# Kernel tuning notes

Hardware: AMD Instinct MI355X
Metric: run time of the kernel (lower is better)

## Reference

```python
import jax, jax.numpy as jnp
import numpy as np

NE = 14          # NUM_ELEMENTS
NC = 20          # NUM_CHANNEL
DEN = NE         # density channel
GRV = NE + 1     # gravity channel

# (id, density, gravity) per element, in id order
_ELEMS = [(0,1,1),(1,4,0),(2,3,1),(3,2,1),(4,0,1),(5,4,0),(6,4,0),(7,0,1),(8,4,0),(9,3,1),(10,3,1),(11,2,1),(12,3,1),(13,4,0)]

def _elem_table():
    t = np.zeros((NE, NC), dtype=np.float32)
    for eid, dens, grav in _ELEMS:
        t[eid, eid] = 1.0
        t[eid, DEN] = dens
        t[eid, GRV] = grav
    return jnp.asarray(t)

# torch.roll semantics: get_above(x)[h] = x[h-1] (wrap)
above = lambda x: jnp.roll(x, 1, axis=2)
below = lambda x: jnp.roll(x, -1, axis=2)
left  = lambda x: jnp.roll(x, 1, axis=3)
right = lambda x: jnp.roll(x, -1, axis=3)

def interp2(sa, sb, if_false, if_a, if_b):
    # faithful to torch: (~a & ~b)*f + a*xa + b*xb (bools broadcast-multiply floats)
    return (jnp.logical_and(~sa, ~sb)) * if_false + sa * if_a + sb * if_b

def setup_inputs() -> dict:
    key = jax.random.key(0)
    k1, k2 = jax.random.split(key)
    B, H, W = 8, 512, 512
    ids = jax.random.randint(k1, (B, H, W), 0, NE)
    world = _elem_table()[ids]                 # [B,H,W,NC]
    world = jnp.transpose(world, (0, 3, 1, 2)) # [B,NC,H,W]
    rand_movement = jax.random.uniform(k2, (B, 1, H, W), dtype=jnp.float32)
    return {"world": world, "rand_movement": rand_movement}

def reference(world, rand_movement):
    B, C, H, W = world.shape
    # --- stone support check (conv2d with zero padding, taps at top-left/top-right) ---
    stone = world[:, 9:10]
    p = jnp.pad(stone, ((0, 0), (0, 0), (1, 1), (1, 1)))
    supports = p[:, :, 0:H, 0:W] + p[:, :, 0:H, 2:W + 2]  # stone[h-1,w-1]+stone[h-1,w+1]
    new_grav = (1.0 - stone) * world[:, GRV:GRV + 1] + stone * (supports < 2)
    world = world.at[:, GRV:GRV + 1].set(new_grav)

    # --- vertical gravity passes over densities 0..3 ---
    did_gravity = jnp.zeros((B, 1, H, W), dtype=world.dtype)
    for curr_density in (0, 1, 2, 3):
        density = world[:, DEN:DEN + 1]
        is_density_above_greater = (above(density) - density) > 0
        is_density_below_less = below(is_density_above_greater)
        is_density_current = density == curr_density
        is_density_above_current = above(is_density_current)
        is_gravity = world[:, GRV:GRV + 1] == 1
        is_cb_gravity = jnp.logical_and(below(is_gravity), is_gravity)
        is_ca_gravity = jnp.logical_and(above(is_gravity), is_gravity)
        does_become_below = is_density_current & is_density_below_less & is_cb_gravity
        does_become_above = is_density_above_greater & is_density_above_current & is_ca_gravity
        did_gravity = did_gravity + does_become_above
        world = interp2(does_become_below, does_become_above, world, below(world), above(world))

    # --- diagonal fall for sand (2) and dust (12) ---
    for elem in (2, 12):
        fall_dir = rand_movement > 0.5
        not_did_gravity = did_gravity <= 0
        for fall_left in (True, False):
            g_dir = left if fall_left else right
            g_not = right if fall_left else left
            is_element = world[:, elem:elem + 1] == 1
            is_ar_element = g_not(above(is_element))
            density = world[:, DEN:DEN + 1]
            is_matching_fall = fall_dir if fall_left else ~fall_dir
            is_ar_matching_fall = g_not(above(is_matching_fall))
            is_bl_density_lower = (density - g_dir(below(density))) > 0
            is_ar_density_higher = (g_not(above(density)) - density) > 0
            is_gravity = world[:, GRV:GRV + 1] == 1
            is_bl_gravity = jnp.logical_and(g_dir(below(is_gravity)), is_gravity)
            is_ar_gravity = jnp.logical_and(g_not(above(is_gravity)), is_gravity)
            ndg_bl = jnp.logical_and(g_dir(below(not_did_gravity)), not_did_gravity)
            ndg_ar = jnp.logical_and(g_not(above(not_did_gravity)), not_did_gravity)
            does_become_bl = is_element & ndg_bl & is_matching_fall & is_bl_density_lower & is_bl_gravity
            does_become_ar = is_ar_element & ndg_ar & is_ar_matching_fall & is_ar_density_higher & is_ar_gravity
            world = interp2(does_become_bl, does_become_ar, world, g_dir(below(world)), g_not(above(world)))
    return world
```

## Files before the change

kernel.cpp:

```cpp
#include <hip/hip_runtime.h>
#include <stdint.h>

#define HH 512
#define WW 512
#define PLANE (HH*WW)
#define NCH 20

#define GRAV_PACK 0x1E9Du

__device__ __forceinline__ void bar_lds() {
    __builtin_amdgcn_sched_barrier(0);
    asm volatile("s_waitcnt lgkmcnt(0)" ::: "memory");
    __builtin_amdgcn_s_barrier();
    __builtin_amdgcn_sched_barrier(0);
}

__device__ __forceinline__ uint32_t eqz4(uint32_t x) {
    uint32_t nz = (x | (x >> 1) | (x >> 2) | (x >> 3)) & 0x01010101u;
    return nz ^ 0x01010101u;
}
__device__ __forceinline__ uint32_t bmask(uint32_t b) {
    uint32_t h = b << 7;
    return (h - (h >> 7)) | h;
}

__device__ __forceinline__ uint32_t pack_cell(float d_,
                                              float c1_, float c5_, float c6_, float c8_,
                                              float c2_, float c9_, float c10_,
                                              float c3_, float c4_) {
    int d = (int)d_;
    int e;
    if (d == 4)      e = (c1_ != 0.f) ? 1 : (c5_ != 0.f) ? 5 : (c6_ != 0.f) ? 6 : (c8_ != 0.f) ? 8 : 13;
    else if (d == 3) e = (c2_ != 0.f) ? 2 : (c9_ != 0.f) ? 9 : (c10_ != 0.f) ? 10 : 12;
    else if (d == 2) e = (c3_ != 0.f) ? 3 : 11;
    else if (d == 1) e = 0;
    else             e = (c4_ != 0.f) ? 4 : 7;
    int g = (int)((GRAV_PACK >> e) & 1u);
    return (uint32_t)(e | (g << 4) | (d << 5));
}

__global__ __launch_bounds__(256) void extract_k(const float* __restrict__ world,
                                                 uint32_t* __restrict__ st) {
    int idx = blockIdx.x * 256 + threadIdx.x;
    int b  = idx >> 16;
    int p4 = idx & 0xFFFF;
    const float4* base = (const float4*)(world + (size_t)b * NCH * PLANE) + p4;
    float4 vD  = base[14 * (PLANE / 4)];
    float4 v1  = base[ 1 * (PLANE / 4)];
    float4 v5  = base[ 5 * (PLANE / 4)];
    float4 v6  = base[ 6 * (PLANE / 4)];
    float4 v8  = base[ 8 * (PLANE / 4)];
    float4 v2  = base[ 2 * (PLANE / 4)];
    float4 v9  = base[ 9 * (PLANE / 4)];
    float4 v10 = base[10 * (PLANE / 4)];
    float4 v3  = base[ 3 * (PLANE / 4)];
    float4 v4  = base[ 4 * (PLANE / 4)];
    uint32_t b0 = pack_cell(vD.x, v1.x, v5.x, v6.x, v8.x, v2.x, v9.x, v10.x, v3.x, v4.x);
    uint32_t b1 = pack_cell(vD.y, v1.y, v5.y, v6.y, v8.y, v2.y, v9.y, v10.y, v3.y, v4.y);
    uint32_t b2 = pack_cell(vD.z, v1.z, v5.z, v6.z, v8.z, v2.z, v9.z, v10.z, v3.z, v4.z);
    uint32_t b3 = pack_cell(vD.w, v1.w, v5.w, v6.w, v8.w, v2.w, v9.w, v10.w, v3.w, v4.w);
    st[idx] = b0 | (b1 << 8) | (b2 << 16) | (b3 << 24);
}

#define TILE_R 32
#define TILE_C 64
#define HALO_T 9
#define HALO_B 8
#define HALO_W 8
#define RH (TILE_R + HALO_T + HALO_B)
#define RWW 20
#define RWS 21
#define NW (RH*RWW)
#define NT 512
#define NOWN 2

__global__ __launch_bounds__(NT, 4) void sim_k(const uint8_t* __restrict__ st_in,
                                               const float* __restrict__ rnd,
                                               float* __restrict__ out) {
    __shared__ uint32_t bufA[RH * RWS];
    __shared__ uint32_t bufB[RH * RWS];
    __shared__ uint32_t aux [RH * RWS];

    const int tid = threadIdx.x;
    const int h0  = blockIdx.y * TILE_R;
    const int w0  = blockIdx.x * TILE_C;

    uint32_t sreg[NOWN], freg[NOWN], dgreg[NOWN];

    auto stage = [&](const uint8_t* stb, const float* rb) {
#pragma unroll
        for (int k = 0; k < NOWN; ++k) {
            int r = tid + k * NT;
            if (r < NW) {
                int i = r / RWW, jw = r - i * RWW;
                int gh  = (h0 + i - HALO_T) & (HH - 1);
                int gwb = (w0 + jw * 4 - HALO_W) & (WW - 1);
                uint32_t w = *(const uint32_t*)(stb + gh * WW + gwb);
                bufA[i * RWS + jw] = w;
                sreg[k] = w;
                float4 rv = *(const float4*)(rb + gh * WW + gwb);
                uint32_t aw = 0;
                aw |= (rv.x > 0.5f) ? 0x00000001u : 0u;
                aw |= (rv.y > 0.5f) ? 0x00000100u : 0u;
                aw |= (rv.z > 0.5f) ? 0x00010000u : 0u;
                aw |= (rv.w > 0.5f) ? 0x01000000u : 0u;
                freg[k] = aw;
                dgreg[k] = 0u;
            }
        }
    };

    auto passes = [&]() {
#pragma unroll
        for (int k = 0; k < NOWN; ++k) {
            int r = tid + k * NT;
            if (r < NW) {
                int i = r / RWW, jw = r - i * RWW;
                uint32_t s = sreg[k];
                uint32_t stm = eqz4((s & 0x0F0F0F0Fu) ^ 0x09090909u);
                int im = (i > 0) ? i - 1 : 0;
                int jl = (jw > 0) ? jw - 1 : 0;
                int jr = (jw < RWW - 1) ? jw + 1 : RWW - 1;
                uint32_t wU  = bufA[im * RWS + jw];
                uint32_t wUL = bufA[im * RWS + jl];
                uint32_t wUR = bufA[im * RWS + jr];
                uint32_t upL = (wU << 8) | (wUL >> 24);
                uint32_t upR = (wU >> 8) | (wUR << 24);
                uint32_t stL = eqz4((upL & 0x0F0F0F0Fu) ^ 0x09090909u);
                uint32_t stR = eqz4((upR & 0x0F0F0F0Fu) ^ 0x09090909u);
                int gh  = (h0 + i - HALO_T) & (HH - 1);
                int gwb = (w0 + jw * 4 - HALO_W) & (WW - 1);
                uint32_t rowOK = (gh != 0) ? 0x01010101u : 0u;
                uint32_t okL = 0x01010101u ^ ((gwb == 0)      ? 0x00000001u : 0u);
                uint32_t okR = 0x01010101u ^ ((gwb == WW - 4) ? 0x01000000u : 0u);
                uint32_t supL = stL & okL & rowOK;
                uint32_t supR = stR & okR & rowOK;
                uint32_t g2 = 0x01010101u ^ (supL & supR);
                uint32_t ns = (s & ~0x10101010u) | (g2 << 4);
                uint32_t res = s ^ ((s ^ ns) & bmask(stm));
                bufB[i * RWS + jw] = res;
                sreg[k] = res;
            }
        }
        bar_lds();

        uint32_t* cur = bufB;
        uint32_t* nxt = bufA;

#pragma unroll
        for (int curr = 0; curr < 4; ++curr) {
            const uint32_t crep = (uint32_t)curr * 0x01010101u;
            const uint32_t CKP7 = crep + 0x0F0F0F0Fu;
#pragma unroll
            for (int k = 0; k < NOWN; ++k) {
                int r = tid + k * NT;
                if (r < NW) {
                    int i = r / RWW, jw = r - i * RWW;
                    int ia = (i > 0) ? i - 1 : 0;
                    int ib = (i < RH - 1) ? i + 1 : RH - 1;
                    uint32_t s  = sreg[k];
                    uint32_t sa = cur[ia * RWS + jw];
                    uint32_t sb = cur[ib * RWS + jw];
                    uint32_t d  = (s  >> 5) & 0x07070707u;
                    uint32_t da = (sa >> 5) & 0x07070707u;
                    uint32_t db = (sb >> 5) & 0x07070707u;
                    uint32_t g  = (s  >> 4) & 0x01010101u;
                    uint32_t ga = (sa >> 4) & 0x01010101u;
                    uint32_t gb = (sb >> 4) & 0x01010101u;
                    uint32_t bel = eqz4(d ^ crep)  & (((CKP7 - db) & 0x10101010u) >> 4) & gb & g;
                    uint32_t abv = eqz4(da ^ crep) & (((CKP7 - d)  & 0x10101010u) >> 4) & ga & g;
                    uint32_t res = s ^ ((s ^ sb) & bmask(bel)) ^ ((s ^ sa) & bmask(abv));
                    nxt[i * RWS + jw] = res;
                    sreg[k] = res;
                    dgreg[k] |= abv;
                    if (curr == 3)
                        aux[i * RWS + jw] = freg[k] | (dgreg[k] << 1);
                }
            }
            bar_lds();
            uint32_t* t = cur; cur = nxt; nxt = t;
        }

#pragma unroll
        for (int pass = 0; pass < 4; ++pass) {
            const int  elem = (pass < 2) ? 2 : 12;
            const bool fl   = ((pass & 1) == 0);
            const uint32_t erep = (uint32_t)elem * 0x01010101u;
#pragma unroll
            for (int k = 0; k < NOWN; ++k) {
                int r = tid + k * NT;
                if (r < NW) {
                    int i = r / RWW, jw = r - i * RWW;
                    int ia = (i > 0) ? i - 1 : 0;
                    int ib = (i < RH - 1) ? i + 1 : RH - 1;
                    int jl = (jw > 0) ? jw - 1 : 0;
                    int jr = (jw < RWW - 1) ? jw + 1 : RWW - 1;
                    uint32_t s  = sreg[k];
                    uint32_t wB = cur[ib * RWS + jw];
                    uint32_t wA = cur[ia * RWS + jw];
                    uint32_t aB = aux[ib * RWS + jw];
                    uint32_t aA = aux[ia * RWS + jw];
                    uint32_t sbl, sar, abl, aar;
                    if (fl) {
                        uint32_t wBL = cur[ib * RWS + jl], wAR = cur[ia * RWS + jr];
                        uint32_t aBL = aux[ib * RWS + jl], aAR = aux[ia * RWS + jr];
                        sbl = (wB << 8) | (wBL >> 24);
                        sar = (wA >> 8) | (wAR << 24);
                        abl = (aB << 8) | (aBL >> 24);
                        aar = (aA >> 8) | (aAR << 24);
                    } else {
                        uint32_t wBR = cur[ib * RWS + jr], wAL = cur[ia * RWS + jl];
                        uint32_t aBR = aux[ib * RWS + jr], aAL = aux[ia * RWS + jl];
                        sbl = (wB >> 8) | (wBR << 24);
                        sar = (wA << 8) | (wAL >> 24);
                        abl = (aB >> 8) | (aBR << 24);
                        aar = (aA << 8) | (aAL >> 24);
                    }
                    uint32_t d   = (s   >> 5) & 0x07070707u;
                    uint32_t dbl = (sbl >> 5) & 0x07070707u;
                    uint32_t dar = (sar >> 5) & 0x07070707u;
                    uint32_t g   = (s   >> 4) & 0x01010101u;
                    uint32_t gbl = (sbl >> 4) & 0x01010101u;
                    uint32_t gar = (sar >> 4) & 0x01010101u;
                    uint32_t ndg   = dgreg[k] ^ 0x01010101u;
                    uint32_t ndgbl = ((~abl) >> 1) & 0x01010101u;
                    uint32_t ndgar = ((~aar) >> 1) & 0x01010101u;
                    uint32_t mtc = (fl ? freg[k] : ~freg[k]) & 0x01010101u;
                    uint32_t mta = (fl ? aar : ~aar) & 0x01010101u;
                    uint32_t eqe  = eqz4((s   & 0x0F0F0F0Fu) ^ erep);
                    uint32_t eqer = eqz4((sar & 0x0F0F0F0Fu) ^ erep);
                    uint32_t bbl = eqe  & ndgbl & ndg & mtc & (((0x12121212u - dbl) & 0x10101010u) >> 4) & gbl & g;
                    uint32_t bar = eqer & ndgar & ndg & mta & (((0x12121212u - d)   & 0x10101010u) >> 4) & gar & g;
                    uint32_t res = s ^ ((s ^ sbl) & bmask(bbl)) ^ ((s ^ sar) & bmask(bar));
                    nxt[i * RWS + jw] = res;
                    sreg[k] = res;
                }
            }
            bar_lds();
            uint32_t* t = cur; cur = nxt; nxt = t;
        }
    };

    auto expand = [&](float* ob, uint32_t w) {
        float* base = ob + (size_t)(h0 + (tid >> 4)) * WW + (w0 + (tid & 15) * 4);
        uint32_t oh0 = 1u << ( w        & 15u);
        uint32_t oh1 = 1u << ((w >>  8) & 15u);
        uint32_t oh2 = 1u << ((w >> 16) & 15u);
        uint32_t oh3 = 1u << ((w >> 24) & 15u);
#pragma unroll
        for (int c = 0; c < 14; ++c) {
            float4 v;
            v.x = (float)((oh0 >> c) & 1u);
            v.y = (float)((oh1 >> c) & 1u);
            v.z = (float)((oh2 >> c) & 1u);
            v.w = (float)((oh3 >> c) & 1u);
            *(float4*)(base + (size_t)c * PLANE) = v;
        }
        float4 vd = { (float)((w >>  5) & 7u), (float)((w >> 13) & 7u),
                      (float)((w >> 21) & 7u), (float)((w >> 29) & 7u) };
        *(float4*)(base + (size_t)14 * PLANE) = vd;
        float4 vg = { (float)((w >>  4) & 1u), (float)((w >> 12) & 1u),
                      (float)((w >> 20) & 1u), (float)((w >> 28) & 1u) };
        *(float4*)(base + (size_t)15 * PLANE) = vg;
        float4 z = {0.f, 0.f, 0.f, 0.f};
#pragma unroll
        for (int c = 16; c < 20; ++c)
            *(float4*)(base + (size_t)c * PLANE) = z;
    };

    const int bA = blockIdx.z, bB = blockIdx.z + 4;
    const uint8_t* stA = st_in + (size_t)bA * PLANE;
    const uint8_t* stB = st_in + (size_t)bB * PLANE;
    const float*   rA  = rnd   + (size_t)bA * PLANE;
    const float*   rB  = rnd   + (size_t)bB * PLANE;
    float* obA = out + (size_t)bA * NCH * PLANE;
    float* obB = out + (size_t)bB * NCH * PLANE;

    const int coreIdx = (HALO_T + (tid >> 4)) * RWS + (HALO_W / 4) + (tid & 15);

    stage(stA, rA);
    bar_lds();
    passes();

    uint32_t wA = bufB[coreIdx];
    stage(stB, rB);
    expand(obA, wA);
    bar_lds();
    passes();

    expand(obB, bufB[coreIdx]);
}

extern "C" void kernel_launch(void* const* d_in, const int* in_sizes, int n_in,
                              void* d_out, int out_size, void* d_ws, size_t ws_size,
                              hipStream_t stream) {
    const float* world = (const float*)d_in[0];
    const float* rnd   = (const float*)d_in[1];
    float* out = (float*)d_out;
    uint32_t* st = (uint32_t*)d_ws;

    extract_k<<<2048, 256, 0, stream>>>(world, st);

    dim3 grid(WW / TILE_C, HH / TILE_R, 4);
    sim_k<<<grid, NT, 0, stream>>>((const uint8_t*)st, rnd, out);
}
```

Before: 55.49 us.

## Fuse float-to-packed extraction into sim kernel and double tile height

Removes the separate extract kernel and its packed intermediate buffer. The sim kernel now reads the ten needed float channels directly from the world tensor during staging and packs them in-register. To reduce the redundant halo reads this causes (halo cells now cost ten float4 loads each), the tile height goes from 32 to 64 rows, with 4 owned words per thread and occupancy bounds lowered to 2 blocks per SIMD group. This saves one launch and a global round trip, but adds more global traffic per halo cell, more registers and fewer resident blocks.

After: 73.89 us. 1.33x slower.

```diff
diff --git a/kernel.cpp b/kernel.cpp
--- a/kernel.cpp
+++ b/kernel.cpp
@@ -39,30 +39,7 @@
     return (uint32_t)(e | (g << 4) | (d << 5));
 }
 
-__global__ __launch_bounds__(256) void extract_k(const float* __restrict__ world,
-                                                 uint32_t* __restrict__ st) {
-    int idx = blockIdx.x * 256 + threadIdx.x;
-    int b  = idx >> 16;
-    int p4 = idx & 0xFFFF;
-    const float4* base = (const float4*)(world + (size_t)b * NCH * PLANE) + p4;
-    float4 vD  = base[14 * (PLANE / 4)];
-    float4 v1  = base[ 1 * (PLANE / 4)];
-    float4 v5  = base[ 5 * (PLANE / 4)];
-    float4 v6  = base[ 6 * (PLANE / 4)];
-    float4 v8  = base[ 8 * (PLANE / 4)];
-    float4 v2  = base[ 2 * (PLANE / 4)];
-    float4 v9  = base[ 9 * (PLANE / 4)];
-    float4 v10 = base[10 * (PLANE / 4)];
-    float4 v3  = base[ 3 * (PLANE / 4)];
-    float4 v4  = base[ 4 * (PLANE / 4)];
-    uint32_t b0 = pack_cell(vD.x, v1.x, v5.x, v6.x, v8.x, v2.x, v9.x, v10.x, v3.x, v4.x);
-    uint32_t b1 = pack_cell(vD.y, v1.y, v5.y, v6.y, v8.y, v2.y, v9.y, v10.y, v3.y, v4.y);
-    uint32_t b2 = pack_cell(vD.z, v1.z, v5.z, v6.z, v8.z, v2.z, v9.z, v10.z, v3.z, v4.z);
-    uint32_t b3 = pack_cell(vD.w, v1.w, v5.w, v6.w, v8.w, v2.w, v9.w, v10.w, v3.w, v4.w);
-    st[idx] = b0 | (b1 << 8) | (b2 << 16) | (b3 << 24);
-}
-
-#define TILE_R 32
+#define TILE_R 64
 #define TILE_C 64
 #define HALO_T 9
 #define HALO_B 8
@@ -72,9 +49,10 @@
 #define RWS 21
 #define NW (RH*RWW)
 #define NT 512
-#define NOWN 2
-
-__global__ __launch_bounds__(NT, 4) void sim_k(const uint8_t* __restrict__ st_in,
+#define NOWN 4
+#define NCORE (TILE_R * 16)
+
+__global__ __launch_bounds__(NT, 2) void sim_k(const float* __restrict__ world,
                                                const float* __restrict__ rnd,
                                                float* __restrict__ out) {
     __shared__ uint32_t bufA[RH * RWS];
@@ -87,7 +65,7 @@
 
     uint32_t sreg[NOWN], freg[NOWN], dgreg[NOWN];
 
-    auto stage = [&](const uint8_t* stb, const float* rb) {
+    auto stage = [&](const float* wb, const float* rb) {
 #pragma unroll
         for (int k = 0; k < NOWN; ++k) {
             int r = tid + k * NT;
@@ -95,10 +73,25 @@
                 int i = r / RWW, jw = r - i * RWW;
                 int gh  = (h0 + i - HALO_T) & (HH - 1);
                 int gwb = (w0 + jw * 4 - HALO_W) & (WW - 1);
-                uint32_t w = *(const uint32_t*)(stb + gh * WW + gwb);
+                const float* cell = wb + gh * WW + gwb;
+                float4 vD  = *(const float4*)(cell + (size_t)14 * PLANE);
+                float4 v1  = *(const float4*)(cell + (size_t) 1 * PLANE);
+                float4 v5  = *(const float4*)(cell + (size_t) 5 * PLANE);
+                float4 v6  = *(const float4*)(cell + (size_t) 6 * PLANE);
+                float4 v8  = *(const float4*)(cell + (size_t) 8 * PLANE);
+                float4 v2  = *(const float4*)(cell + (size_t) 2 * PLANE);
+                float4 v9  = *(const float4*)(cell + (size_t) 9 * PLANE);
+                float4 v10 = *(const float4*)(cell + (size_t)10 * PLANE);
+                float4 v3  = *(const float4*)(cell + (size_t) 3 * PLANE);
+                float4 v4  = *(const float4*)(cell + (size_t) 4 * PLANE);
+                float4 rv  = *(const float4*)(rb + gh * WW + gwb);
+                uint32_t b0 = pack_cell(vD.x, v1.x, v5.x, v6.x, v8.x, v2.x, v9.x, v10.x, v3.x, v4.x);
+                uint32_t b1 = pack_cell(vD.y, v1.y, v5.y, v6.y, v8.y, v2.y, v9.y, v10.y, v3.y, v4.y);
+                uint32_t b2 = pack_cell(vD.z, v1.z, v5.z, v6.z, v8.z, v2.z, v9.z, v10.z, v3.z, v4.z);
+                uint32_t b3 = pack_cell(vD.w, v1.w, v5.w, v6.w, v8.w, v2.w, v9.w, v10.w, v3.w, v4.w);
+                uint32_t w = b0 | (b1 << 8) | (b2 << 16) | (b3 << 24);
                 bufA[i * RWS + jw] = w;
                 sreg[k] = w;
-                float4 rv = *(const float4*)(rb + gh * WW + gwb);
                 uint32_t aw = 0;
                 aw |= (rv.x > 0.5f) ? 0x00000001u : 0u;
                 aw |= (rv.y > 0.5f) ? 0x00000100u : 0u;
@@ -218,7 +211,6 @@
                     }
                     uint32_t d   = (s   >> 5) & 0x07070707u;
                     uint32_t dbl = (sbl >> 5) & 0x07070707u;
-                    uint32_t dar = (sar >> 5) & 0x07070707u;
                     uint32_t g   = (s   >> 4) & 0x01010101u;
                     uint32_t gbl = (sbl >> 4) & 0x01010101u;
                     uint32_t gar = (sar >> 4) & 0x01010101u;
@@ -241,8 +233,8 @@
         }
     };
 
-    auto expand = [&](float* ob, uint32_t w) {
-        float* base = ob + (size_t)(h0 + (tid >> 4)) * WW + (w0 + (tid & 15) * 4);
+    auto expand1 = [&](float* ob, uint32_t w, int ci) {
+        float* base = ob + (size_t)(h0 + (ci >> 4)) * WW + (w0 + (ci & 15) * 4);
         uint32_t oh0 = 1u << ( w        & 15u);
         uint32_t oh1 = 1u << ((w >>  8) & 15u);
         uint32_t oh2 = 1u << ((w >> 16) & 15u);
@@ -269,26 +261,31 @@
     };
 
     const int bA = blockIdx.z, bB = blockIdx.z + 4;
-    const uint8_t* stA = st_in + (size_t)bA * PLANE;
-    const uint8_t* stB = st_in + (size_t)bB * PLANE;
-    const float*   rA  = rnd   + (size_t)bA * PLANE;
-    const float*   rB  = rnd   + (size_t)bB * PLANE;
+    const float* wbA = world + (size_t)bA * NCH * PLANE;
+    const float* wbB = world + (size_t)bB * NCH * PLANE;
+    const float* rA  = rnd   + (size_t)bA * PLANE;
+    const float* rB  = rnd   + (size_t)bB * PLANE;
     float* obA = out + (size_t)bA * NCH * PLANE;
     float* obB = out + (size_t)bB * NCH * PLANE;
 
-    const int coreIdx = (HALO_T + (tid >> 4)) * RWS + (HALO_W / 4) + (tid & 15);
-
-    stage(stA, rA);
+    auto coreOf = [&](int ci) {
+        return (HALO_T + (ci >> 4)) * RWS + (HALO_W / 4) + (ci & 15);
+    };
+
+    stage(wbA, rA);
     bar_lds();
     passes();
 
-    uint32_t wA = bufB[coreIdx];
-    stage(stB, rB);
-    expand(obA, wA);
+    uint32_t wA0 = bufB[coreOf(tid)];
+    uint32_t wA1 = bufB[coreOf(tid + NT)];
+    stage(wbB, rB);
+    expand1(obA, wA0, tid);
+    expand1(obA, wA1, tid + NT);
     bar_lds();
     passes();
 
-    expand(obB, bufB[coreIdx]);
+    expand1(obB, bufB[coreOf(tid)], tid);
+    expand1(obB, bufB[coreOf(tid + NT)], tid + NT);
 }
 
 extern "C" void kernel_launch(void* const* d_in, const int* in_sizes, int n_in,
@@ -297,10 +294,7 @@
     const float* world = (const float*)d_in[0];
     const float* rnd   = (const float*)d_in[1];
     float* out = (float*)d_out;
-    uint32_t* st = (uint32_t*)d_ws;
-
-    extract_k<<<2048, 256, 0, stream>>>(world, st);
 
     dim3 grid(WW / TILE_C, HH / TILE_R, 4);
-    sim_k<<<grid, NT, 0, stream>>>((const uint8_t*)st, rnd, out);
-}
+    sim_k<<<grid, NT, 0, stream>>>(world, rnd, out);
+}
```

## Switch to full-width row tiles, dropping horizontal halo and wrapping columns in LDS

Applied to the files above, without the earlier changes.

Each block now covers 8 full 512-wide rows instead of a 32x64 tile. Horizontal halo is gone because column wrap is handled by masking indices within the 128-word LDS row. This leaves only the vertical halo, 17 rows per 8 core rows, which is a larger vertical-halo ratio than before. Random-number loads are now limited to rows near the core, and the divide/modulo index math becomes shifts. The trade-off is 7 cells per thread, more registers, a lower occupancy hint and more redundant vertical-halo compute.

Measured after the change: 67.15 us. 1.21x slower.

```diff
diff --git a/kernel.cpp b/kernel.cpp
--- a/kernel.cpp
+++ b/kernel.cpp
@@ -62,28 +62,24 @@
     st[idx] = b0 | (b1 << 8) | (b2 << 16) | (b3 << 24);
 }
 
-#define TILE_R 32
-#define TILE_C 64
+#define TILE_R 8
 #define HALO_T 9
 #define HALO_B 8
-#define HALO_W 8
 #define RH (TILE_R + HALO_T + HALO_B)
-#define RWW 20
-#define RWS 21
+#define RWW 128
 #define NW (RH*RWW)
 #define NT 512
-#define NOWN 2
-
-__global__ __launch_bounds__(NT, 4) void sim_k(const uint8_t* __restrict__ st_in,
+#define NOWN 7
+
+__global__ __launch_bounds__(NT, 2) void sim_k(const uint8_t* __restrict__ st_in,
                                                const float* __restrict__ rnd,
                                                float* __restrict__ out) {
-    __shared__ uint32_t bufA[RH * RWS];
-    __shared__ uint32_t bufB[RH * RWS];
-    __shared__ uint32_t aux [RH * RWS];
+    __shared__ uint32_t bufA[NW];
+    __shared__ uint32_t bufB[NW];
+    __shared__ uint32_t aux [NW];
 
     const int tid = threadIdx.x;
-    const int h0  = blockIdx.y * TILE_R;
-    const int w0  = blockIdx.x * TILE_C;
+    const int h0  = blockIdx.x * TILE_R;
 
     uint32_t sreg[NOWN], freg[NOWN], dgreg[NOWN];
 
@@ -92,18 +88,19 @@
         for (int k = 0; k < NOWN; ++k) {
             int r = tid + k * NT;
             if (r < NW) {
-                int i = r / RWW, jw = r - i * RWW;
-                int gh  = (h0 + i - HALO_T) & (HH - 1);
-                int gwb = (w0 + jw * 4 - HALO_W) & (WW - 1);
-                uint32_t w = *(const uint32_t*)(stb + gh * WW + gwb);
-                bufA[i * RWS + jw] = w;
+                int i = r >> 7, jw = r & 127;
+                int gh = (h0 + i - HALO_T) & (HH - 1);
+                uint32_t w = *(const uint32_t*)(stb + gh * WW + jw * 4);
+                bufA[r] = w;
                 sreg[k] = w;
-                float4 rv = *(const float4*)(rb + gh * WW + gwb);
                 uint32_t aw = 0;
-                aw |= (rv.x > 0.5f) ? 0x00000001u : 0u;
-                aw |= (rv.y > 0.5f) ? 0x00000100u : 0u;
-                aw |= (rv.z > 0.5f) ? 0x00010000u : 0u;
-                aw |= (rv.w > 0.5f) ? 0x01000000u : 0u;
+                if (i >= HALO_T - 4 && i < RH - HALO_B + 4) {
+                    float4 rv = *(const float4*)(rb + gh * WW + jw * 4);
+                    aw |= (rv.x > 0.5f) ? 0x00000001u : 0u;
+                    aw |= (rv.y > 0.5f) ? 0x00000100u : 0u;
+                    aw |= (rv.z > 0.5f) ? 0x00010000u : 0u;
+                    aw |= (rv.w > 0.5f) ? 0x01000000u : 0u;
+                }
                 freg[k] = aw;
                 dgreg[k] = 0u;
             }
@@ -115,30 +112,29 @@
         for (int k = 0; k < NOWN; ++k) {
             int r = tid + k * NT;
             if (r < NW) {
-                int i = r / RWW, jw = r - i * RWW;
+                int i = r >> 7, jw = r & 127;
                 uint32_t s = sreg[k];
                 uint32_t stm = eqz4((s & 0x0F0F0F0Fu) ^ 0x09090909u);
-                int im = (i > 0) ? i - 1 : 0;
-                int jl = (jw > 0) ? jw - 1 : 0;
-                int jr = (jw < RWW - 1) ? jw + 1 : RWW - 1;
-                uint32_t wU  = bufA[im * RWS + jw];
-                uint32_t wUL = bufA[im * RWS + jl];
-                uint32_t wUR = bufA[im * RWS + jr];
+                int ibase = (i > 0) ? (r - RWW - jw) : (r - jw);
+                int jl = (jw + 127) & 127;
+                int jr = (jw + 1) & 127;
+                uint32_t wU  = bufA[ibase + jw];
+                uint32_t wUL = bufA[ibase + jl];
+                uint32_t wUR = bufA[ibase + jr];
                 uint32_t upL = (wU << 8) | (wUL >> 24);
                 uint32_t upR = (wU >> 8) | (wUR << 24);
                 uint32_t stL = eqz4((upL & 0x0F0F0F0Fu) ^ 0x09090909u);
                 uint32_t stR = eqz4((upR & 0x0F0F0F0Fu) ^ 0x09090909u);
-                int gh  = (h0 + i - HALO_T) & (HH - 1);
-                int gwb = (w0 + jw * 4 - HALO_W) & (WW - 1);
+                int gh = (h0 + i - HALO_T) & (HH - 1);
                 uint32_t rowOK = (gh != 0) ? 0x01010101u : 0u;
-                uint32_t okL = 0x01010101u ^ ((gwb == 0)      ? 0x00000001u : 0u);
-                uint32_t okR = 0x01010101u ^ ((gwb == WW - 4) ? 0x01000000u : 0u);
+                uint32_t okL = 0x01010101u ^ ((jw == 0)       ? 0x00000001u : 0u);
+                uint32_t okR = 0x01010101u ^ ((jw == RWW - 1) ? 0x01000000u : 0u);
                 uint32_t supL = stL & okL & rowOK;
                 uint32_t supR = stR & okR & rowOK;
                 uint32_t g2 = 0x01010101u ^ (supL & supR);
                 uint32_t ns = (s & ~0x10101010u) | (g2 << 4);
                 uint32_t res = s ^ ((s ^ ns) & bmask(stm));
-                bufB[i * RWS + jw] = res;
+                bufB[r] = res;
                 sreg[k] = res;
             }
         }
@@ -155,12 +151,12 @@
             for (int k = 0; k < NOWN; ++k) {
                 int r = tid + k * NT;
                 if (r < NW) {
-                    int i = r / RWW, jw = r - i * RWW;
-                    int ia = (i > 0) ? i - 1 : 0;
-                    int ib = (i < RH - 1) ? i + 1 : RH - 1;
+                    int i = r >> 7;
+                    int ra = (i > 0)      ? r - RWW : r;
+                    int rb = (i < RH - 1) ? r + RWW : r;
                     uint32_t s  = sreg[k];
-                    uint32_t sa = cur[ia * RWS + jw];
-                    uint32_t sb = cur[ib * RWS + jw];
+                    uint32_t sa = cur[ra];
+                    uint32_t sb = cur[rb];
                     uint32_t d  = (s  >> 5) & 0x07070707u;
                     uint32_t da = (sa >> 5) & 0x07070707u;
                     uint32_t db = (sb >> 5) & 0x07070707u;
@@ -170,11 +166,11 @@
                     uint32_t bel = eqz4(d ^ crep)  & (((CKP7 - db) & 0x10101010u) >> 4) & gb & g;
                     uint32_t abv = eqz4(da ^ crep) & (((CKP7 - d)  & 0x10101010u) >> 4) & ga & g;
                     uint32_t res = s ^ ((s ^ sb) & bmask(bel)) ^ ((s ^ sa) & bmask(abv));
-                    nxt[i * RWS + jw] = res;
+                    nxt[r] = res;
                     sreg[k] = res;
                     dgreg[k] |= abv;
                     if (curr == 3)
-                        aux[i * RWS + jw] = freg[k] | (dgreg[k] << 1);
+                        aux[r] = freg[k] | (dgreg[k] << 1);
                 }
             }
             bar_lds();
@@ -190,27 +186,27 @@
             for (int k = 0; k < NOWN; ++k) {
                 int r = tid + k * NT;
                 if (r < NW) {
-                    int i = r / RWW, jw = r - i * RWW;
-                    int ia = (i > 0) ? i - 1 : 0;
-                    int ib = (i < RH - 1) ? i + 1 : RH - 1;
-                    int jl = (jw > 0) ? jw - 1 : 0;
-                    int jr = (jw < RWW - 1) ? jw + 1 : RWW - 1;
+                    int i = r >> 7, jw = r & 127;
+                    int iab = ((i > 0)      ? (i - 1) : i) * RWW;
+                    int ibb = ((i < RH - 1) ? (i + 1) : i) * RWW;
+                    int jl = (jw + 127) & 127;
+                    int jr = (jw + 1) & 127;
                     uint32_t s  = sreg[k];
-                    uint32_t wB = cur[ib * RWS + jw];
-                    uint32_t wA = cur[ia * RWS + jw];
-                    uint32_t aB = aux[ib * RWS + jw];
-                    uint32_t aA = aux[ia * RWS + jw];
+                    uint32_t wB = cur[ibb + jw];
+                    uint32_t wA = cur[iab + jw];
+                    uint32_t aB = aux[ibb + jw];
+                    uint32_t aA = aux[iab + jw];
                     uint32_t sbl, sar, abl, aar;
                     if (fl) {
-                        uint32_t wBL = cur[ib * RWS + jl], wAR = cur[ia * RWS + jr];
-                        uint32_t aBL = aux[ib * RWS + jl], aAR = aux[ia * RWS + jr];
+                        uint32_t wBL = cur[ibb + jl], wAR = cur[iab + jr];
+                        uint32_t aBL = aux[ibb + jl], aAR = aux[iab + jr];
                         sbl = (wB << 8) | (wBL >> 24);
                         sar = (wA >> 8) | (wAR << 24);
                         abl = (aB << 8) | (aBL >> 24);
                         aar = (aA >> 8) | (aAR << 24);
                     } else {
-                        uint32_t wBR = cur[ib * RWS + jr], wAL = cur[ia * RWS + jl];
-                        uint32_t aBR = aux[ib * RWS + jr], aAL = aux[ia * RWS + jl];
+                        uint32_t wBR = cur[ibb + jr], wAL = cur[iab + jl];
+                        uint32_t aBR = aux[ibb + jr], aAL = aux[iab + jl];
                         sbl = (wB >> 8) | (wBR << 24);
                         sar = (wA << 8) | (wAL >> 24);
                         abl = (aB >> 8) | (aBR << 24);
@@ -218,7 +214,6 @@
                     }
                     uint32_t d   = (s   >> 5) & 0x07070707u;
                     uint32_t dbl = (sbl >> 5) & 0x07070707u;
-                    uint32_t dar = (sar >> 5) & 0x07070707u;
                     uint32_t g   = (s   >> 4) & 0x01010101u;
                     uint32_t gbl = (sbl >> 4) & 0x01010101u;
                     uint32_t gar = (sar >> 4) & 0x01010101u;
@@ -232,7 +227,7 @@
                     uint32_t bbl = eqe  & ndgbl & ndg & mtc & (((0x12121212u - dbl) & 0x10101010u) >> 4) & gbl & g;
                     uint32_t bar = eqer & ndgar & ndg & mta & (((0x12121212u - d)   & 0x10101010u) >> 4) & gar & g;
                     uint32_t res = s ^ ((s ^ sbl) & bmask(bbl)) ^ ((s ^ sar) & bmask(bar));
-                    nxt[i * RWS + jw] = res;
+                    nxt[r] = res;
                     sreg[k] = res;
                 }
             }
@@ -241,8 +236,8 @@
         }
     };
 
-    auto expand = [&](float* ob, uint32_t w) {
-        float* base = ob + (size_t)(h0 + (tid >> 4)) * WW + (w0 + (tid & 15) * 4);
+    auto expand1 = [&](float* ob, uint32_t w, int ci) {
+        float* base = ob + (size_t)(h0 + (ci >> 7)) * WW + (ci & 127) * 4;
         uint32_t oh0 = 1u << ( w        & 15u);
         uint32_t oh1 = 1u << ((w >>  8) & 15u);
         uint32_t oh2 = 1u << ((w >> 16) & 15u);
@@ -268,7 +263,7 @@
             *(float4*)(base + (size_t)c * PLANE) = z;
     };
 
-    const int bA = blockIdx.z, bB = blockIdx.z + 4;
+    const int bA = blockIdx.y, bB = blockIdx.y + 4;
     const uint8_t* stA = st_in + (size_t)bA * PLANE;
     const uint8_t* stB = st_in + (size_t)bB * PLANE;
     const float*   rA  = rnd   + (size_t)bA * PLANE;
@@ -276,19 +271,23 @@
     float* obA = out + (size_t)bA * NCH * PLANE;
     float* obB = out + (size_t)bB * NCH * PLANE;
 
-    const int coreIdx = (HALO_T + (tid >> 4)) * RWS + (HALO_W / 4) + (tid & 15);
+    const int core0 = tid + HALO_T * RWW;
+    const int core1 = tid + NT + HALO_T * RWW;
 
     stage(stA, rA);
     bar_lds();
     passes();
 
-    uint32_t wA = bufB[coreIdx];
+    uint32_t wA0 = bufB[core0];
+    uint32_t wA1 = bufB[core1];
     stage(stB, rB);
-    expand(obA, wA);
+    expand1(obA, wA0, tid);
+    expand1(obA, wA1, tid + NT);
     bar_lds();
     passes();
 
-    expand(obB, bufB[coreIdx]);
+    expand1(obB, bufB[core0], tid);
+    expand1(obB, bufB[core1], tid + NT);
 }
 
 extern "C" void kernel_launch(void* const* d_in, const int* in_sizes, int n_in,
@@ -301,6 +300,6 @@
 
     extract_k<<<2048, 256, 0, stream>>>(world, st);
 
-    dim3 grid(WW / TILE_C, HH / TILE_R, 4);
+    dim3 grid(HH / TILE_R, 4, 1);
     sim_k<<<grid, NT, 0, stream>>>((const uint8_t*)st, rnd, out);
 }
```

## Fuse extract and simulation into one kernel with per-batch flag synchronisation

Applied to the files above, without the earlier changes.

Merges the separate channel-packing kernel into the simulation kernel. Each group of 64 blocks packs one batch image, then waits on a global atomic counter until the whole image is packed before simulating two adjacent column tiles. Later groups are gated on the completion of the group LEAD batches earlier, so packing of later batches can overlap simulation and output writes of earlier ones. This removes a kernel boundary and lets the two phases overlap. In exchange it adds a memset launch, depends on enough co-resident blocks to avoid spin-wait deadlock, and adds atomic and fence overhead.

After: 190.0 us. 242% more time.

```diff
diff --git a/kernel.cpp b/kernel.cpp
--- a/kernel.cpp
+++ b/kernel.cpp
@@ -5,7 +5,6 @@
 #define WW 512
 #define PLANE (HH*WW)
 #define NCH 20
-
 #define GRAV_PACK 0x1E9Du
 
 __device__ __forceinline__ void bar_lds() {
@@ -39,29 +38,6 @@
     return (uint32_t)(e | (g << 4) | (d << 5));
 }
 
-__global__ __launch_bounds__(256) void extract_k(const float* __restrict__ world,
-                                                 uint32_t* __restrict__ st) {
-    int idx = blockIdx.x * 256 + threadIdx.x;
-    int b  = idx >> 16;
-    int p4 = idx & 0xFFFF;
-    const float4* base = (const float4*)(world + (size_t)b * NCH * PLANE) + p4;
-    float4 vD  = base[14 * (PLANE / 4)];
-    float4 v1  = base[ 1 * (PLANE / 4)];
-    float4 v5  = base[ 5 * (PLANE / 4)];
-    float4 v6  = base[ 6 * (PLANE / 4)];
-    float4 v8  = base[ 8 * (PLANE / 4)];
-    float4 v2  = base[ 2 * (PLANE / 4)];
-    float4 v9  = base[ 9 * (PLANE / 4)];
-    float4 v10 = base[10 * (PLANE / 4)];
-    float4 v3  = base[ 3 * (PLANE / 4)];
-    float4 v4  = base[ 4 * (PLANE / 4)];
-    uint32_t b0 = pack_cell(vD.x, v1.x, v5.x, v6.x, v8.x, v2.x, v9.x, v10.x, v3.x, v4.x);
-    uint32_t b1 = pack_cell(vD.y, v1.y, v5.y, v6.y, v8.y, v2.y, v9.y, v10.y, v3.y, v4.y);
-    uint32_t b2 = pack_cell(vD.z, v1.z, v5.z, v6.z, v8.z, v2.z, v9.z, v10.z, v3.z, v4.z);
-    uint32_t b3 = pack_cell(vD.w, v1.w, v5.w, v6.w, v8.w, v2.w, v9.w, v10.w, v3.w, v4.w);
-    st[idx] = b0 | (b1 << 8) | (b2 << 16) | (b3 << 24);
-}
-
 #define TILE_R 32
 #define TILE_C 64
 #define HALO_T 9
@@ -73,21 +49,78 @@
 #define NW (RH*RWW)
 #define NT 512
 #define NOWN 2
-
-__global__ __launch_bounds__(NT, 4) void sim_k(const uint8_t* __restrict__ st_in,
-                                               const float* __restrict__ rnd,
-                                               float* __restrict__ out) {
+#define LEAD 4
+
+__global__ __launch_bounds__(NT, 4) void fused_k(const float* __restrict__ world,
+                                                 const float* __restrict__ rnd,
+                                                 float* __restrict__ out,
+                                                 uint32_t* __restrict__ st,
+                                                 uint32_t* __restrict__ eflag,
+                                                 uint32_t* __restrict__ sflag) {
     __shared__ uint32_t bufA[RH * RWS];
     __shared__ uint32_t bufB[RH * RWS];
     __shared__ uint32_t aux [RH * RWS];
 
     const int tid = threadIdx.x;
-    const int h0  = blockIdx.y * TILE_R;
-    const int w0  = blockIdx.x * TILE_C;
+    const int g   = blockIdx.x >> 6;
+    const int m   = blockIdx.x & 63;
+
+    if (g >= LEAD) {
+        if (tid == 0)
+            while (__hip_atomic_load(&sflag[g - LEAD], __ATOMIC_RELAXED,
+                                     __HIP_MEMORY_SCOPE_AGENT) < 64u)
+                __builtin_amdgcn_s_sleep(8);
+        __syncthreads();
+    }
+
+    {
+        const float* wb = world + (size_t)g * NCH * PLANE;
+        uint32_t* stw = st + (size_t)g * (PLANE / 4);
+#pragma unroll
+        for (int q = 0; q < 2; ++q) {
+            int widx = m * 1024 + q * 512 + tid;
+            const float4* base = (const float4*)wb + widx;
+            float4 vD  = base[14 * (PLANE / 4)];
+            float4 v1  = base[ 1 * (PLANE / 4)];
+            float4 v5  = base[ 5 * (PLANE / 4)];
+            float4 v6  = base[ 6 * (PLANE / 4)];
+            float4 v8  = base[ 8 * (PLANE / 4)];
+            float4 v2  = base[ 2 * (PLANE / 4)];
+            float4 v9  = base[ 9 * (PLANE / 4)];
+            float4 v10 = base[10 * (PLANE / 4)];
+            float4 v3  = base[ 3 * (PLANE / 4)];
+            float4 v4  = base[ 4 * (PLANE / 4)];
+            uint32_t b0 = pack_cell(vD.x, v1.x, v5.x, v6.x, v8.x, v2.x, v9.x, v10.x, v3.x, v4.x);
+            uint32_t b1 = pack_cell(vD.y, v1.y, v5.y, v6.y, v8.y, v2.y, v9.y, v10.y, v3.y, v4.y);
+            uint32_t b2 = pack_cell(vD.z, v1.z, v5.z, v6.z, v8.z, v2.z, v9.z, v10.z, v3.z, v4.z);
+            uint32_t b3 = pack_cell(vD.w, v1.w, v5.w, v6.w, v8.w, v2.w, v9.w, v10.w, v3.w, v4.w);
+            uint32_t w = b0 | (b1 << 8) | (b2 << 16) | (b3 << 24);
+            __hip_atomic_store(&stw[widx], w, __ATOMIC_RELAXED, __HIP_MEMORY_SCOPE_AGENT);
+        }
+    }
+    __threadfence();
+    __syncthreads();
+    if (tid == 0) {
+        __hip_atomic_fetch_add(&eflag[g], 1u, __ATOMIC_RELEASE, __HIP_MEMORY_SCOPE_AGENT);
+        while (__hip_atomic_load(&eflag[g], __ATOMIC_ACQUIRE,
+                                 __HIP_MEMORY_SCOPE_AGENT) < 64u)
+            __builtin_amdgcn_s_sleep(8);
+        __threadfence();
+    }
+    __syncthreads();
+
+    const uint8_t* stb = (const uint8_t*)(st + (size_t)g * (PLANE / 4));
+    const float*   rb  = rnd + (size_t)g * PLANE;
+    float*         ob  = out + (size_t)g * NCH * PLANE;
+
+    const int tloc = m * 2;
+    const int h0   = (tloc >> 3) * TILE_R;
+    const int w0A  = (tloc & 7) * TILE_C;
+    const int w0B  = w0A + TILE_C;
 
     uint32_t sreg[NOWN], freg[NOWN], dgreg[NOWN];
 
-    auto stage = [&](const uint8_t* stb, const float* rb) {
+    auto stage = [&](int w0) {
 #pragma unroll
         for (int k = 0; k < NOWN; ++k) {
             int r = tid + k * NT;
@@ -110,7 +143,7 @@
         }
     };
 
-    auto passes = [&]() {
+    auto passes = [&](int w0) {
 #pragma unroll
         for (int k = 0; k < NOWN; ++k) {
             int r = tid + k * NT;
@@ -164,11 +197,11 @@
                     uint32_t d  = (s  >> 5) & 0x07070707u;
                     uint32_t da = (sa >> 5) & 0x07070707u;
                     uint32_t db = (sb >> 5) & 0x07070707u;
-                    uint32_t g  = (s  >> 4) & 0x01010101u;
+                    uint32_t gg = (s  >> 4) & 0x01010101u;
                     uint32_t ga = (sa >> 4) & 0x01010101u;
                     uint32_t gb = (sb >> 4) & 0x01010101u;
-                    uint32_t bel = eqz4(d ^ crep)  & (((CKP7 - db) & 0x10101010u) >> 4) & gb & g;
-                    uint32_t abv = eqz4(da ^ crep) & (((CKP7 - d)  & 0x10101010u) >> 4) & ga & g;
+                    uint32_t bel = eqz4(d ^ crep)  & (((CKP7 - db) & 0x10101010u) >> 4) & gb & gg;
+                    uint32_t abv = eqz4(da ^ crep) & (((CKP7 - d)  & 0x10101010u) >> 4) & ga & gg;
                     uint32_t res = s ^ ((s ^ sb) & bmask(bel)) ^ ((s ^ sa) & bmask(abv));
                     nxt[i * RWS + jw] = res;
                     sreg[k] = res;
@@ -218,8 +251,7 @@
                     }
                     uint32_t d   = (s   >> 5) & 0x07070707u;
                     uint32_t dbl = (sbl >> 5) & 0x07070707u;
-                    uint32_t dar = (sar >> 5) & 0x07070707u;
-                    uint32_t g   = (s   >> 4) & 0x01010101u;
+                    uint32_t gg  = (s   >> 4) & 0x01010101u;
                     uint32_t gbl = (sbl >> 4) & 0x01010101u;
                     uint32_t gar = (sar >> 4) & 0x01010101u;
                     uint32_t ndg   = dgreg[k] ^ 0x01010101u;
@@ -229,8 +261,8 @@
                     uint32_t mta = (fl ? aar : ~aar) & 0x01010101u;
                     uint32_t eqe  = eqz4((s   & 0x0F0F0F0Fu) ^ erep);
                     uint32_t eqer = eqz4((sar & 0x0F0F0F0Fu) ^ erep);
-                    uint32_t bbl = eqe  & ndgbl & ndg & mtc & (((0x12121212u - dbl) & 0x10101010u) >> 4) & gbl & g;
-                    uint32_t bar = eqer & ndgar & ndg & mta & (((0x12121212u - d)   & 0x10101010u) >> 4) & gar & g;
+                    uint32_t bbl = eqe  & ndgbl & ndg & mtc & (((0x12121212u - dbl) & 0x10101010u) >> 4) & gbl & gg;
+                    uint32_t bar = eqer & ndgar & ndg & mta & (((0x12121212u - d)   & 0x10101010u) >> 4) & gar & gg;
                     uint32_t res = s ^ ((s ^ sbl) & bmask(bbl)) ^ ((s ^ sar) & bmask(bar));
                     nxt[i * RWS + jw] = res;
                     sreg[k] = res;
@@ -241,7 +273,7 @@
         }
     };
 
-    auto expand = [&](float* ob, uint32_t w) {
+    auto expand1 = [&](int w0, uint32_t w) {
         float* base = ob + (size_t)(h0 + (tid >> 4)) * WW + (w0 + (tid & 15) * 4);
         uint32_t oh0 = 1u << ( w        & 15u);
         uint32_t oh1 = 1u << ((w >>  8) & 15u);
@@ -268,27 +300,21 @@
             *(float4*)(base + (size_t)c * PLANE) = z;
     };
 
-    const int bA = blockIdx.z, bB = blockIdx.z + 4;
-    const uint8_t* stA = st_in + (size_t)bA * PLANE;
-    const uint8_t* stB = st_in + (size_t)bB * PLANE;
-    const float*   rA  = rnd   + (size_t)bA * PLANE;
-    const float*   rB  = rnd   + (size_t)bB * PLANE;
-    float* obA = out + (size_t)bA * NCH * PLANE;
-    float* obB = out + (size_t)bB * NCH * PLANE;
-
     const int coreIdx = (HALO_T + (tid >> 4)) * RWS + (HALO_W / 4) + (tid & 15);
 
-    stage(stA, rA);
+    stage(w0A);
     bar_lds();
-    passes();
+    passes(w0A);
 
     uint32_t wA = bufB[coreIdx];
-    stage(stB, rB);
-    expand(obA, wA);
+    stage(w0B);
+    expand1(w0A, wA);
     bar_lds();
-    passes();
-
-    expand(obB, bufB[coreIdx]);
+    passes(w0B);
+
+    if (tid == 0)
+        __hip_atomic_fetch_add(&sflag[g], 1u, __ATOMIC_RELAXED, __HIP_MEMORY_SCOPE_AGENT);
+    expand1(w0B, bufB[coreIdx]);
 }
 
 extern "C" void kernel_launch(void* const* d_in, const int* in_sizes, int n_in,
@@ -297,10 +323,11 @@
     const float* world = (const float*)d_in[0];
     const float* rnd   = (const float*)d_in[1];
     float* out = (float*)d_out;
-    uint32_t* st = (uint32_t*)d_ws;
-
-    extract_k<<<2048, 256, 0, stream>>>(world, st);
-
-    dim3 grid(WW / TILE_C, HH / TILE_R, 4);
-    sim_k<<<grid, NT, 0, stream>>>((const uint8_t*)st, rnd, out);
-}
+    uint32_t* st    = (uint32_t*)d_ws;
+    uint32_t* eflag = (uint32_t*)((char*)d_ws + 2 * 1024 * 1024);
+    uint32_t* sflag = eflag + 8;
+
+    hipMemsetAsync(eflag, 0, 64, stream);
+
+    fused_k<<<512, NT, 0, stream>>>(world, rnd, out, st, eflag, sflag);
+}
```
